# Optimization experiments

Hardware: AMD Instinct MI355X
Metric: run time of the kernel (lower is better)

Reference implementation:

```python
import jax, jax.numpy as jnp
import numpy as np
from jax import lax

B, P, ENC, H, A, E, V, TC = 64, 196, 2048, 1024, 1024, 512, 10000, 32


def setup_inputs() -> dict:
    key = jax.random.key(0)
    ks = jax.random.split(key, 24)
    s = 0.02
    inp = {
        'enc_out': jax.random.normal(ks[0], (B, P, ENC), jnp.float32),
        'enc_captions': jax.random.randint(ks[1], (B, TC), 0, V),
        'lengths': jax.random.randint(ks[2], (B,), 2, TC + 1).at[0].set(TC),
        'W_enc_att': jax.random.normal(ks[3], (A, ENC)) * s,
        'b_enc_att': jnp.zeros((A,)),
        'W_dec_att': jax.random.normal(ks[4], (A, H)) * s,
        'b_dec_att': jnp.zeros((A,)),
        'W_full': jax.random.normal(ks[5], (1, A)) * s,
        'b_full': jnp.zeros((1,)),
        'emb': jax.random.uniform(ks[6], (V, E), minval=-0.1, maxval=0.1),
        'W_ih': jax.random.normal(ks[7], (4 * H, E + ENC)) * s,
        'b_ih': jnp.zeros((4 * H,)),
        'W_hh': jax.random.normal(ks[8], (4 * H, H)) * s,
        'b_hh': jnp.zeros((4 * H,)),
        'W_init_h': jax.random.normal(ks[9], (H, ENC)) * s,
        'b_init_h': jnp.zeros((H,)),
        'W_init_c': jax.random.normal(ks[10], (H, ENC)) * s,
        'b_init_c': jnp.zeros((H,)),
        'W_beta': jax.random.normal(ks[11], (ENC, H)) * s,
        'b_beta': jnp.zeros((ENC,)),
        'W_fc': jax.random.uniform(ks[12], (V, H), minval=-0.1, maxval=0.1),
        'b_fc': jnp.zeros((V,)),
    }
    return inp


def reference(enc_out, enc_captions, lengths,
              W_enc_att, b_enc_att, W_dec_att, b_dec_att, W_full, b_full,
              emb, W_ih, b_ih, W_hh, b_hh,
              W_init_h, b_init_h, W_init_c, b_init_c,
              W_beta, b_beta, W_fc, b_fc):
    T = enc_captions.shape[1] - 1  # static max decode length (setup forces one full-length row)
    ind = jnp.argsort(-lengths)
    lens = lengths[ind]
    eo = enc_out[ind]              # [B,P,ENC] sorted by length desc
    caps = enc_captions[ind]
    dec_lens = lens - 1
    embs = emb[caps]               # [B,TC,E]

    mean_a = eo.mean(axis=1)
    h0 = mean_a @ W_init_h.T + b_init_h
    c0 = mean_a @ W_init_c.T + b_init_c

    # encoder projection is time-invariant; hoist out of the loop
    enc_att = jnp.einsum('bpe,ae->bpa', eo, W_enc_att) + b_enc_att  # [B,P,A]

    mask_ts = jnp.arange(T)[:, None] < dec_lens[None, :]            # [T,B]
    emb_ts = jnp.swapaxes(embs[:, :T, :], 0, 1)                     # [T,B,E]

    def step(carry, xs):
        h, c = carry
        emb_t, m = xs  # [B,E], [B] bool (active rows = leading batch_size_t)
        # attention
        dec = h @ W_dec_att.T + b_dec_att                            # [B,A]
        a = jax.nn.relu(enc_att + dec[:, None, :]) @ W_full[0] + b_full[0]  # [B,P]
        alpha = jax.nn.softmax(a, axis=1)
        context = jnp.einsum('bpe,bp->be', eo, alpha)                # [B,ENC]
        # gate + LSTM cell (torch gate order: i, f, g, o)
        gate = jax.nn.sigmoid(h @ W_beta.T + b_beta)
        awe = gate * context
        x = jnp.concatenate([emb_t, awe], axis=1)
        gates = x @ W_ih.T + b_ih + h @ W_hh.T + b_hh
        i, f, g, o = jnp.split(gates, 4, axis=1)
        c_new = jax.nn.sigmoid(f) * c + jax.nn.sigmoid(i) * jnp.tanh(g)
        h_new = jax.nn.sigmoid(o) * jnp.tanh(c_new)
        m2 = m[:, None]
        h2 = jnp.where(m2, h_new, h)  # inactive rows keep frozen state
        c2 = jnp.where(m2, c_new, c)
        mf = m2.astype(h.dtype)
        preds = (h_new @ W_fc.T + b_fc) * mf  # dropout = identity (eval)
        return (h2, c2), (preds, alpha * mf)

    (_, _), (preds, alphas) = lax.scan(step, (h0, c0), (emb_ts, mask_ts))
    predictions = jnp.swapaxes(preds, 0, 1)   # [B,T,V]
    alphas = jnp.swapaxes(alphas, 0, 1)       # [B,T,P]
    return predictions, alphas, caps, dec_lens, ind
```

## Files before the change

### kernel.cpp

```cpp
#include <hip/hip_runtime.h>

#define Bn   64
#define Pp   196
#define ENCd 2048
#define Hd   1024
#define Ad   1024
#define Ed   512
#define Vd   10000
#define TCd  32
#define Td   31
#define XHW  3584
#define VPAD 10240

typedef short bf16x8 __attribute__((ext_vector_type(8)));
typedef float f32x4  __attribute__((ext_vector_type(4)));

static __device__ __forceinline__ float bf2f(unsigned short u) {
    unsigned int x = ((unsigned int)u) << 16;
    float f; __builtin_memcpy(&f, &x, 4); return f;
}
static __device__ __forceinline__ unsigned short f2bf(float f) {
    unsigned int x; __builtin_memcpy(&x, &f, 4);
    x += 0x7fffu + ((x >> 16) & 1u);
    return (unsigned short)(x >> 16);
}
static __device__ __forceinline__ float sigf(float x) { return 1.f / (1.f + expf(-x)); }


__global__ void sort_kernel(const int* __restrict__ lengths, const int* __restrict__ captions,
                            int* __restrict__ ind, int* __restrict__ dl,
                            float* __restrict__ out_caps, float* __restrict__ out_dl,
                            float* __restrict__ out_ind) {
    __shared__ int s_ind[Bn];
    int tid = threadIdx.x;
    int Lt = lengths[tid];
    int pos = 0;
    for (int k = 0; k < Bn; ++k) {
        int Lk = lengths[k];
        pos += (Lk > Lt) || (Lk == Lt && k < tid);
    }
    s_ind[pos] = tid;
    __syncthreads();
    int src = s_ind[tid];
    ind[tid] = src;
    int d = lengths[src] - 1;
    dl[tid] = d;
    out_ind[tid] = (float)src;
    out_dl[tid] = (float)d;
    for (int j = 0; j < TCd; ++j)
        out_caps[tid * TCd + j] = (float)captions[src * TCd + j];
}

__global__ void cvt_kernel(const float* __restrict__ src, unsigned short* __restrict__ dst, int n) {
    int i = blockIdx.x * 256 + threadIdx.x;
    int stride = gridDim.x * 256;
    for (; i < n; i += stride) dst[i] = f2bf(src[i]);
}

__global__ void wcat_kernel(const float* __restrict__ wih, const float* __restrict__ whh,
                            unsigned short* __restrict__ wcat) {
    int j = blockIdx.y;
    int idx = blockIdx.x * 256 + threadIdx.x;
    float v = (idx < 2560) ? wih[(size_t)j * 2560 + idx] : whh[(size_t)j * 1024 + (idx - 2560)];
    wcat[(size_t)j * XHW + idx] = f2bf(v);
}

__global__ void biascat_kernel(const float* __restrict__ bih, const float* __restrict__ bhh,
                               float* __restrict__ bc) {
    int i = blockIdx.x * 256 + threadIdx.x;
    bc[i] = bih[i] + bhh[i];
}

__global__ void gather_eo_kernel(const float* __restrict__ enc_out, const int* __restrict__ ind,
                                 unsigned short* __restrict__ eo) {
    int b = blockIdx.y;
    int idx = blockIdx.x * 256 + threadIdx.x;
    int src = ind[b];
    eo[(size_t)b * (Pp * ENCd) + idx] = f2bf(enc_out[(size_t)src * (Pp * ENCd) + idx]);
}

__global__ void mean_kernel(const float* __restrict__ enc_out, const int* __restrict__ ind,
                            float* __restrict__ meanf) {
    int b = blockIdx.y;
    int e = blockIdx.x * 256 + threadIdx.x;
    int src = ind[b];
    const float* base = enc_out + (size_t)src * (Pp * ENCd) + e;
    float s = 0.f;
    for (int p = 0; p < Pp; ++p) s += base[(size_t)p * ENCd];
    meanf[b * ENCd + e] = s * (1.f / 196.f);
}

__global__ void embs_kernel(const float* __restrict__ emb, const int* __restrict__ captions,
                            const int* __restrict__ ind, unsigned short* __restrict__ xhbuf) {
    int b = blockIdx.y;
    int idx = blockIdx.x * 256 + threadIdx.x;
    int t = idx >> 9, e = idx & 511;
    int src = ind[b];
    int cap = captions[src * TCd + t];
    xhbuf[((size_t)t * Bn + b) * XHW + e] = f2bf(emb[(size_t)cap * Ed + e]);
}

__global__ void init_hc_kernel(const float* __restrict__ meanf,
                               const float* __restrict__ winh, const float* __restrict__ binh,
                               const float* __restrict__ winc, const float* __restrict__ binc,
                               unsigned short* __restrict__ xh0, float* __restrict__ cbuf) {
    int id = blockIdx.x * 256 + threadIdx.x;
    int n = id & 2047;
    int m = id >> 11;
    bool is_c = n >= 1024;
    int nn = is_c ? n - 1024 : n;
    const float* wrow = (is_c ? winc : winh) + (size_t)nn * ENCd;
    const float* arow = meanf + (size_t)m * ENCd;
    float acc = is_c ? binc[nn] : binh[nn];
    const float4* w4 = (const float4*)wrow;
    const float4* a4 = (const float4*)arow;
    for (int k = 0; k < ENCd / 4; ++k) {
        float4 wv = w4[k], av = a4[k];
        acc += wv.x * av.x + wv.y * av.y + wv.z * av.z + wv.w * av.w;
    }
    if (is_c) cbuf[(size_t)m * Hd + nn] = acc;
    else      xh0[(size_t)m * XHW + 2560 + nn] = f2bf(acc);
}

template<int MT, int NT, int EPI>
__global__ __launch_bounds__(256)
void gemm_mn(const unsigned short* __restrict__ A, int lda,
             const unsigned short* __restrict__ W,
             const float* __restrict__ bias,
             int N, int nsup, int nb, int K,
             float* __restrict__ outf, unsigned short* __restrict__ outb, int ldo,
             const int* __restrict__ dl) {
    int wave = threadIdx.x >> 6, lane = threadIdx.x & 63;
    int mt = blockIdx.x / nb;
    int nt = (blockIdx.x % nb) * 4 + wave;
    if (nt >= nsup) return;
    int m0 = mt * (MT * 16);
    int n0 = nt * (NT * 16);
    int col = lane & 15, quad = lane >> 4;

    const unsigned short* aptr = A + (size_t)(m0 + col) * lda + quad * 8;
    const unsigned short* wptr = W + (size_t)(n0 + col) * K + quad * 8;

    f32x4 acc[MT * NT];
#pragma unroll
    for (int i = 0; i < MT * NT; ++i) acc[i] = (f32x4){0.f, 0.f, 0.f, 0.f};

    for (int k = 0; k < K; k += 32) {
        bf16x8 wf[NT];
#pragma unroll
        for (int j = 0; j < NT; ++j)
            wf[j] = *(const bf16x8*)(wptr + (size_t)j * 16 * K + k);
#pragma unroll
        for (int mi = 0; mi < MT; ++mi) {
            bf16x8 af = *(const bf16x8*)(aptr + (size_t)mi * 16 * lda + k);
#pragma unroll
            for (int j = 0; j < NT; ++j)
                acc[mi * NT + j] = __builtin_amdgcn_mfma_f32_16x16x32_bf16(af, wf[j], acc[mi * NT + j], 0, 0, 0);
        }
    }

#pragma unroll
    for (int mi = 0; mi < MT; ++mi) {
#pragma unroll
        for (int r = 0; r < 4; ++r) {
            int m = m0 + mi * 16 + quad * 4 + r;
            if (EPI == 5 && m >= Td * Bn) continue;
#pragma unroll
            for (int j = 0; j < NT; ++j) {
                int n = n0 + j * 16 + col;
                if (EPI == 1) {
                    outb[(size_t)m * ldo + n] = f2bf(acc[mi * NT + j][r] + bias[n]);
                } else {
                    if (n < N) {
                        int t = m >> 6, b = m & 63;
                        float mf = (t < dl[b]) ? 1.f : 0.f;
                        float v = acc[mi * NT + j][r] + bias[n];
                        outf[((size_t)b * Td + t) * Vd + n] = v * mf;
                    }
                }
            }
        }
    }
}

template<int SK>
__global__ void gemm_sk4(const unsigned short* __restrict__ A, int lda,
                         const unsigned short* __restrict__ W,
                         int N, int K, float* __restrict__ part) {
    int wid  = (blockIdx.x * 256 + threadIdx.x) >> 6;
    int lane = threadIdx.x & 63;
    int ntiles = N >> 4;
    int s = wid / ntiles;
    int nt = wid - s * ntiles;
    int col = lane & 15, quad = lane >> 4;
    int kLen = K / SK, k0 = s * kLen;

    const unsigned short* aptr = A + (size_t)col * lda + k0 + quad * 8;
    const unsigned short* wptr = W + (size_t)(nt * 16 + col) * K + k0 + quad * 8;

    f32x4 acc[4];
#pragma unroll
    for (int i = 0; i < 4; ++i) acc[i] = (f32x4){0.f, 0.f, 0.f, 0.f};

    for (int k = 0; k < kLen; k += 32) {
        bf16x8 wf = *(const bf16x8*)(wptr + k);
#pragma unroll
        for (int mi = 0; mi < 4; ++mi) {
            bf16x8 af = *(const bf16x8*)(aptr + (size_t)mi * 16 * lda + k);
            acc[mi] = __builtin_amdgcn_mfma_f32_16x16x32_bf16(af, wf, acc[mi], 0, 0, 0);
        }
    }

    int n = nt * 16 + col;
    float* base = part + (size_t)s * Bn * N;
#pragma unroll
    for (int mi = 0; mi < 4; ++mi) {
#pragma unroll
        for (int r = 0; r < 4; ++r) {
            int m = mi * 16 + quad * 4 + r;
            base[(size_t)m * N + n] = acc[mi][r];
        }
    }
}


__global__ void scores_kernel(const float* __restrict__ pdb, const float* __restrict__ bdec,
                              const unsigned short* __restrict__ encatt,
                              const float* __restrict__ wfull,
                              float* __restrict__ scores) {
    int b = blockIdx.y;
    int tid = threadIdx.x;
    __shared__ float sdec[Ad];
    for (int i = tid; i < Ad; i += 256) {
        float v = bdec[i];
#pragma unroll
        for (int s2 = 0; s2 < 4; ++s2) v += pdb[((size_t)(s2 * Bn + b)) * 3072 + i];
        sdec[i] = v;
    }
    __syncthreads();
    int wave = tid >> 6, lane = tid & 63;
    int p = blockIdx.x * 4 + wave;
    const unsigned int* ea = (const unsigned int*)(encatt + ((size_t)(b * Pp + p) << 10));
    const float2* dp = (const float2*)sdec;
    const float2* wf = (const float2*)wfull;
    float acc = 0.f;
#pragma unroll
    for (int it = 0; it < 8; ++it) {
        int i2 = it * 64 + lane;
        unsigned int u = ea[i2];
        float2 dv = dp[i2];
        float2 wv = wf[i2];
        acc += fmaxf(bf2f((unsigned short)(u & 0xffffu)) + dv.x, 0.f) * wv.x;
        acc += fmaxf(bf2f((unsigned short)(u >> 16)) + dv.y, 0.f) * wv.y;
    }
    for (int o2 = 32; o2; o2 >>= 1) acc += __shfl_xor(acc, o2);
    if (lane == 0) scores[b * Pp + p] = acc;
}

__global__ void softmaxctx_kernel(const float* __restrict__ scores,
                                  const float* __restrict__ pdb, const float* __restrict__ bbeta,
                                  const unsigned short* __restrict__ eo,
                                  unsigned short* __restrict__ xh_t,
                                  float* __restrict__ out_alpha,
                                  const int* __restrict__ dl, int t) {
    int b = blockIdx.y, tid = threadIdx.x;
    __shared__ float red[256];
    __shared__ float sal[Pp];
    float s = (tid < Pp) ? scores[b * Pp + tid] : -1e30f;
    red[tid] = s; __syncthreads();
    for (int o2 = 128; o2; o2 >>= 1) { if (tid < o2) red[tid] = fmaxf(red[tid], red[tid + o2]); __syncthreads(); }
    float mx = red[0]; __syncthreads();
    float e = (tid < Pp) ? expf(s - mx) : 0.f;
    red[tid] = e; __syncthreads();
    for (int o2 = 128; o2; o2 >>= 1) { if (tid < o2) red[tid] += red[tid + o2]; __syncthreads(); }
    float inv = 1.f / red[0];
    if (tid < Pp) {
        float a = e * inv;
        sal[tid] = a;
        if (blockIdx.x == 0) {
            float mf = (t < dl[b]) ? 1.f : 0.f;
            out_alpha[((size_t)b * Td + t) * Pp + tid] = a * mf;
        }
    }
    __syncthreads();

    int e0 = blockIdx.x * 512 + tid * 2;
    const unsigned int* base = (const unsigned int*)(eo + (size_t)b * Pp * ENCd);
    int half = e0 >> 1;
    float a0 = 0.f, a1 = 0.f;
    for (int p = 0; p < Pp; ++p) {
        unsigned int u = base[p * (ENCd / 2) + half];
        float w = sal[p];
        a0 += w * bf2f((unsigned short)(u & 0xffffu));
        a1 += w * bf2f((unsigned short)(u >> 16));
    }
    float g0 = bbeta[e0], g1 = bbeta[e0 + 1];
#pragma unroll
    for (int s2 = 0; s2 < 4; ++s2) {
        const float* pb = pdb + ((size_t)(s2 * Bn + b)) * 3072 + Ad + e0;
        g0 += pb[0]; g1 += pb[1];
    }
    g0 = sigf(g0); g1 = sigf(g1);
    xh_t[(size_t)b * XHW + 512 + e0]     = f2bf(a0 * g0);
    xh_t[(size_t)b * XHW + 512 + e0 + 1] = f2bf(a1 * g1);
}

__global__ void lstm_kernel(const float* __restrict__ pg, const float* __restrict__ biascat,
                            float* __restrict__ c,
                            const unsigned short* __restrict__ xh_cur,
                            unsigned short* __restrict__ xh_next,
                            unsigned short* __restrict__ hall, const int* __restrict__ dl, int t) {
    int id = blockIdx.x * 256 + threadIdx.x;
    int b = id >> 10, j = id & 1023;
    float iv = biascat[j], fv = biascat[1024 + j], gv = biascat[2048 + j], ov = biascat[3072 + j];
#pragma unroll
    for (int s2 = 0; s2 < 8; ++s2) {
        const float* base = pg + ((size_t)(s2 * Bn + b)) * 4096;
        iv += base[j]; fv += base[1024 + j]; gv += base[2048 + j]; ov += base[3072 + j];
    }
    float co = c[id];
    float cn = sigf(fv) * co + sigf(iv) * tanhf(gv);
    float hn = sigf(ov) * tanhf(cn);
    bool m = t < dl[b];
    float ho = bf2f(xh_cur[(size_t)b * XHW + 2560 + j]);
    float h2 = m ? hn : ho;
    c[id] = m ? cn : co;
    xh_next[(size_t)b * XHW + 2560 + j] = f2bf(h2);
    hall[((size_t)t * Bn + b) * Hd + j] = f2bf(hn);
}


extern "C" void kernel_launch(void* const* d_in, const int* in_sizes, int n_in,
                              void* d_out, int out_size, void* d_ws, size_t ws_size,
                              hipStream_t stream) {
    const float* enc_out   = (const float*)d_in[0];
    const int*   captions  = (const int*)d_in[1];
    const int*   lengths   = (const int*)d_in[2];
    const float* W_enc_att = (const float*)d_in[3];
    const float* b_enc_att = (const float*)d_in[4];
    const float* W_dec_att = (const float*)d_in[5];
    const float* b_dec_att = (const float*)d_in[6];
    const float* W_full    = (const float*)d_in[7];
    const float* emb       = (const float*)d_in[9];
    const float* W_ih      = (const float*)d_in[10];
    const float* b_ih      = (const float*)d_in[11];
    const float* W_hh      = (const float*)d_in[12];
    const float* b_hh      = (const float*)d_in[13];
    const float* W_init_h  = (const float*)d_in[14];
    const float* b_init_h  = (const float*)d_in[15];
    const float* W_init_c  = (const float*)d_in[16];
    const float* b_init_c  = (const float*)d_in[17];
    const float* W_beta    = (const float*)d_in[18];
    const float* b_beta    = (const float*)d_in[19];
    const float* W_fc      = (const float*)d_in[20];
    const float* b_fc      = (const float*)d_in[21];

    float* out       = (float*)d_out;
    float* out_pred  = out;
    float* out_alpha = out + (size_t)Bn * Td * Vd;
    float* out_caps  = out_alpha + (size_t)Bn * Td * Pp;
    float* out_dl    = out_caps + (size_t)Bn * TCd;
    float* out_ind   = out_dl + Bn;

    char* ws = (char*)d_ws;
    size_t off = 0;
    auto take = [&](size_t n) -> char* {
        char* p = ws + off;
        off = (off + n + 255) & ~(size_t)255;
        return p;
    };
    int* ind_i   = (int*)take(Bn * 4);
    int* dl_i    = (int*)take(Bn * 4);
    unsigned short* eo_b     = (unsigned short*)take((size_t)Bn * Pp * ENCd * 2);
    unsigned short* encatt_b = (unsigned short*)take((size_t)Bn * Pp * Ad * 2);
    unsigned short* wcat_b   = (unsigned short*)take((size_t)4096 * XHW * 2);
    unsigned short* wfc_b    = (unsigned short*)take((size_t)VPAD * Hd * 2);
    unsigned short* wenc_b   = (unsigned short*)take((size_t)Ad * ENCd * 2);
    unsigned short* wdb_b    = (unsigned short*)take((size_t)3072 * Hd * 2);
    float*          biascat  = (float*)take(4096 * 4);
    float*          meanf    = (float*)take((size_t)Bn * ENCd * 4);
    unsigned short* xhbuf    = (unsigned short*)take((size_t)32 * Bn * XHW * 2);
    float*          cbuf     = (float*)take((size_t)Bn * Hd * 4);
    unsigned short* hall     = (unsigned short*)take((size_t)2048 * Hd * 2);
    float*          scores   = (float*)take((size_t)Bn * Pp * 4);
    float*          pdb      = (float*)take((size_t)4 * Bn * 3072 * 4);
    float*          pgates   = (float*)take((size_t)8 * Bn * 4096 * 4);
    (void)ws_size; (void)out_size; (void)n_in; (void)in_sizes;

    sort_kernel<<<1, 64, 0, stream>>>(lengths, captions, ind_i, dl_i, out_caps, out_dl, out_ind);

    auto cvt = [&](const float* s, unsigned short* d, int n) {
        int g = (n + 255) / 256; if (g > 4096) g = 4096;
        cvt_kernel<<<g, 256, 0, stream>>>(s, d, n);
    };
    cvt(W_enc_att, wenc_b, Ad * ENCd);
    cvt(W_dec_att, wdb_b, Ad * Hd);
    cvt(W_beta,  wdb_b + (size_t)Ad * Hd, ENCd * Hd);
    cvt(W_fc,    wfc_b,   Vd * Hd);
    wcat_kernel<<<dim3(14, 4096), 256, 0, stream>>>(W_ih, W_hh, wcat_b);
    biascat_kernel<<<16, 256, 0, stream>>>(b_ih, b_hh, biascat);

    gather_eo_kernel<<<dim3(1568, Bn), 256, 0, stream>>>(enc_out, ind_i, eo_b);
    mean_kernel<<<dim3(8, Bn), 256, 0, stream>>>(enc_out, ind_i, meanf);
    embs_kernel<<<dim3(62, Bn), 256, 0, stream>>>(emb, captions, ind_i, xhbuf);

    init_hc_kernel<<<512, 256, 0, stream>>>(meanf, W_init_h, b_init_h, W_init_c, b_init_c,
                                            xhbuf, cbuf);

    gemm_mn<8, 4, 1><<<98 * 4, 256, 0, stream>>>(eo_b, ENCd, wenc_b, b_enc_att,
        Ad, 16, 4, ENCd, nullptr, encatt_b, Ad, nullptr);

    for (int t = 0; t < Td; ++t) {
        unsigned short* xh_t = xhbuf + (size_t)t * Bn * XHW;
        unsigned short* xh_n = xhbuf + (size_t)(t + 1) * Bn * XHW;

        gemm_sk4<4><<<192, 256, 0, stream>>>(xh_t + 2560, XHW, wdb_b, 3072, Hd, pdb);

        scores_kernel<<<dim3(49, Bn), 256, 0, stream>>>(pdb, b_dec_att, encatt_b, W_full, scores);

        softmaxctx_kernel<<<dim3(4, Bn), 256, 0, stream>>>(scores, pdb, b_beta, eo_b,
            xh_t, out_alpha, dl_i, t);

        gemm_sk4<8><<<512, 256, 0, stream>>>(xh_t, XHW, wcat_b, 4096, XHW, pgates);

        lstm_kernel<<<256, 256, 0, stream>>>(pgates, biascat, cbuf, xh_t, xh_n, hall, dl_i, t);
    }

    gemm_mn<8, 4, 5><<<16 * 40, 256, 0, stream>>>(hall, Hd, wfc_b, b_fc,
        Vd, 157, 40, Hd, out_pred, nullptr, 0, dl_i);
}
```

Before: 2.602 ms.

## Fuse attention scores, softmax and context into one kernel; shrink GEMM M-tile

Merges the per-step scores kernel and the softmax/context kernel into a single 512-thread attention kernel, with two blocks per batch row. Each block recomputes all 196 scores and keeps them in shared memory instead of a global scores buffer, and the softmax reduction now uses wave shuffles. This removes one launch and a global round trip per step, but duplicates the score work and gives far fewer blocks (128 versus 3136 plus 256), which lowers parallelism. Separately, the gemm_mn M-tile drops from 8 to 4 with doubled grids, trading operand reuse for more blocks.

```diff
diff --git a/kernel.cpp b/kernel.cpp
--- a/kernel.cpp
+++ b/kernel.cpp
@@ -122,7 +122,7 @@
     else      xh0[(size_t)m * XHW + 2560 + nn] = f2bf(acc);
 }
 
-template<int MT, int NT, int EPI>
+template<int EPI>
 __global__ __launch_bounds__(256)
 void gemm_mn(const unsigned short* __restrict__ A, int lda,
              const unsigned short* __restrict__ W,
@@ -130,6 +130,7 @@
              int N, int nsup, int nb, int K,
              float* __restrict__ outf, unsigned short* __restrict__ outb, int ldo,
              const int* __restrict__ dl) {
+    const int MT = 4, NT = 4;
     int wave = threadIdx.x >> 6, lane = threadIdx.x & 63;
     int mt = blockIdx.x / nb;
     int nt = (blockIdx.x % nb) * 4 + wave;
@@ -223,73 +224,79 @@
     }
 }
 
-
-__global__ void scores_kernel(const float* __restrict__ pdb, const float* __restrict__ bdec,
-                              const unsigned short* __restrict__ encatt,
-                              const float* __restrict__ wfull,
-                              float* __restrict__ scores) {
+__global__ __launch_bounds__(512)
+void attention_kernel(const float* __restrict__ pdb, const float* __restrict__ bdec,
+                      const float* __restrict__ bbeta,
+                      const unsigned short* __restrict__ encatt,
+                      const float* __restrict__ wfull,
+                      const unsigned short* __restrict__ eo,
+                      unsigned short* __restrict__ xh_t,
+                      float* __restrict__ out_alpha,
+                      const int* __restrict__ dl, int t) {
     int b = blockIdx.y;
+    int half = blockIdx.x;
     int tid = threadIdx.x;
     __shared__ float sdec[Ad];
-    for (int i = tid; i < Ad; i += 256) {
+    __shared__ float sal[Pp];
+    __shared__ float sred[2];
+
+    for (int i = tid; i < Ad; i += 512) {
         float v = bdec[i];
 #pragma unroll
         for (int s2 = 0; s2 < 4; ++s2) v += pdb[((size_t)(s2 * Bn + b)) * 3072 + i];
         sdec[i] = v;
     }
     __syncthreads();
+
     int wave = tid >> 6, lane = tid & 63;
-    int p = blockIdx.x * 4 + wave;
-    const unsigned int* ea = (const unsigned int*)(encatt + ((size_t)(b * Pp + p) << 10));
-    const float2* dp = (const float2*)sdec;
-    const float2* wf = (const float2*)wfull;
-    float acc = 0.f;
-#pragma unroll
-    for (int it = 0; it < 8; ++it) {
-        int i2 = it * 64 + lane;
-        unsigned int u = ea[i2];
-        float2 dv = dp[i2];
-        float2 wv = wf[i2];
-        acc += fmaxf(bf2f((unsigned short)(u & 0xffffu)) + dv.x, 0.f) * wv.x;
-        acc += fmaxf(bf2f((unsigned short)(u >> 16)) + dv.y, 0.f) * wv.y;
-    }
-    for (int o2 = 32; o2; o2 >>= 1) acc += __shfl_xor(acc, o2);
-    if (lane == 0) scores[b * Pp + p] = acc;
-}
-
-__global__ void softmaxctx_kernel(const float* __restrict__ scores,
-                                  const float* __restrict__ pdb, const float* __restrict__ bbeta,
-                                  const unsigned short* __restrict__ eo,
-                                  unsigned short* __restrict__ xh_t,
-                                  float* __restrict__ out_alpha,
-                                  const int* __restrict__ dl, int t) {
-    int b = blockIdx.y, tid = threadIdx.x;
-    __shared__ float red[256];
-    __shared__ float sal[Pp];
-    float s = (tid < Pp) ? scores[b * Pp + tid] : -1e30f;
-    red[tid] = s; __syncthreads();
-    for (int o2 = 128; o2; o2 >>= 1) { if (tid < o2) red[tid] = fmaxf(red[tid], red[tid + o2]); __syncthreads(); }
-    float mx = red[0]; __syncthreads();
-    float e = (tid < Pp) ? expf(s - mx) : 0.f;
-    red[tid] = e; __syncthreads();
-    for (int o2 = 128; o2; o2 >>= 1) { if (tid < o2) red[tid] += red[tid + o2]; __syncthreads(); }
-    float inv = 1.f / red[0];
+    for (int p = wave; p < Pp; p += 8) {
+        const unsigned int* ea = (const unsigned int*)(encatt + ((size_t)(b * Pp + p) << 10));
+        const float2* dp = (const float2*)sdec;
+        const float2* wf = (const float2*)wfull;
+        float acc = 0.f;
+#pragma unroll
+        for (int it = 0; it < 8; ++it) {
+            int i2 = it * 64 + lane;
+            unsigned int u = ea[i2];
+            float2 dv = dp[i2], wv = wf[i2];
+            acc += fmaxf(bf2f((unsigned short)(u & 0xffffu)) + dv.x, 0.f) * wv.x;
+            acc += fmaxf(bf2f((unsigned short)(u >> 16)) + dv.y, 0.f) * wv.y;
+        }
+        for (int o2 = 32; o2; o2 >>= 1) acc += __shfl_xor(acc, o2);
+        if (lane == 0) sal[p] = acc;
+    }
+    __syncthreads();
+
+    if (wave == 0) {
+        float v0 = sal[lane];
+        float v1 = sal[lane + 64];
+        float v2 = sal[lane + 128];
+        float v3 = (lane + 192 < Pp) ? sal[lane + 192] : -1e30f;
+        float mx = fmaxf(fmaxf(v0, v1), fmaxf(v2, v3));
+        for (int o2 = 32; o2; o2 >>= 1) mx = fmaxf(mx, __shfl_xor(mx, o2));
+        float s = expf(v0 - mx) + expf(v1 - mx) + expf(v2 - mx) +
+                  ((lane + 192 < Pp) ? expf(v3 - mx) : 0.f);
+        for (int o2 = 32; o2; o2 >>= 1) s += __shfl_xor(s, o2);
+        if (lane == 0) { sred[0] = mx; sred[1] = 1.f / s; }
+    }
+    __syncthreads();
+    float mx = sred[0], inv = sred[1];
     if (tid < Pp) {
-        float a = e * inv;
+        float a = expf(sal[tid] - mx) * inv;
         sal[tid] = a;
-        if (blockIdx.x == 0) {
+        if (half == 0) {
             float mf = (t < dl[b]) ? 1.f : 0.f;
             out_alpha[((size_t)b * Td + t) * Pp + tid] = a * mf;
         }
     }
     __syncthreads();
 
-    int e0 = blockIdx.x * 512 + tid * 2;
+    int e0 = half * 1024 + tid * 2;
     const unsigned int* base = (const unsigned int*)(eo + (size_t)b * Pp * ENCd);
-    int half = e0 >> 1;
+    int h2i = e0 >> 1;
     float a0 = 0.f, a1 = 0.f;
     for (int p = 0; p < Pp; ++p) {
-        unsigned int u = base[p * (ENCd / 2) + half];
+        unsigned int u = base[(size_t)p * (ENCd / 2) + h2i];
         float w = sal[p];
         a0 += w * bf2f((unsigned short)(u & 0xffffu));
         a1 += w * bf2f((unsigned short)(u >> 16));
@@ -382,7 +389,6 @@
     unsigned short* xhbuf    = (unsigned short*)take((size_t)32 * Bn * XHW * 2);
     float*          cbuf     = (float*)take((size_t)Bn * Hd * 4);
     unsigned short* hall     = (unsigned short*)take((size_t)2048 * Hd * 2);
-    float*          scores   = (float*)take((size_t)Bn * Pp * 4);
     float*          pdb      = (float*)take((size_t)4 * Bn * 3072 * 4);
     float*          pgates   = (float*)take((size_t)8 * Bn * 4096 * 4);
     (void)ws_size; (void)out_size; (void)n_in; (void)in_sizes;
@@ -407,7 +413,7 @@
     init_hc_kernel<<<512, 256, 0, stream>>>(meanf, W_init_h, b_init_h, W_init_c, b_init_c,
                                             xhbuf, cbuf);
 
-    gemm_mn<8, 4, 1><<<98 * 4, 256, 0, stream>>>(eo_b, ENCd, wenc_b, b_enc_att,
+    gemm_mn<1><<<196 * 4, 256, 0, stream>>>(eo_b, ENCd, wenc_b, b_enc_att,
         Ad, 16, 4, ENCd, nullptr, encatt_b, Ad, nullptr);
 
     for (int t = 0; t < Td; ++t) {
@@ -416,16 +422,14 @@
 
         gemm_sk4<4><<<192, 256, 0, stream>>>(xh_t + 2560, XHW, wdb_b, 3072, Hd, pdb);
 
-        scores_kernel<<<dim3(49, Bn), 256, 0, stream>>>(pdb, b_dec_att, encatt_b, W_full, scores);
-
-        softmaxctx_kernel<<<dim3(4, Bn), 256, 0, stream>>>(scores, pdb, b_beta, eo_b,
-            xh_t, out_alpha, dl_i, t);
+        attention_kernel<<<dim3(2, Bn), 512, 0, stream>>>(pdb, b_dec_att, b_beta,
+            encatt_b, W_full, eo_b, xh_t, out_alpha, dl_i, t);
 
         gemm_sk4<8><<<512, 256, 0, stream>>>(xh_t, XHW, wcat_b, 4096, XHW, pgates);
 
         lstm_kernel<<<256, 256, 0, stream>>>(pgates, biascat, cbuf, xh_t, xh_n, hall, dl_i, t);
     }
 
-    gemm_mn<8, 4, 5><<<16 * 40, 256, 0, stream>>>(hall, Hd, wfc_b, b_fc,
+    gemm_mn<5><<<32 * 40, 256, 0, stream>>>(hall, Hd, wfc_b, b_fc,
         Vd, 157, 40, Hd, out_pred, nullptr, 0, dl_i);
 }
```

Measured after the change: 2.739 ms. +5.2%, slower.
